# Kernel tuning notes

Measured on AMD Instinct MI355X. Metric: run time of the kernel, lower is better.

Reference implementation:

```python
import jax, jax.numpy as jnp
import numpy as np

B, S, H = 4, 2048, 1024
NH, HD = 16, 64
FF = 4 * H
EPS = 1e-5


def _layernorm(x, g, b):
    m = jnp.mean(x, axis=-1, keepdims=True)
    v = jnp.mean((x - m) ** 2, axis=-1, keepdims=True)
    return (x - m) * jax.lax.rsqrt(v + EPS) * g + b


def setup_inputs() -> dict:
    key = jax.random.key(0)
    ks = jax.random.split(key, 12)
    std = 1.0 / np.sqrt(H)
    inp = {
        "x": jax.random.normal(ks[0], (B, S, H), dtype=jnp.float32),
        "attention_mask": jnp.ones((B, S), dtype=bool),
        "Wq": jax.random.normal(ks[1], (H, H), dtype=jnp.float32) * std,
        "bq": jnp.zeros((H,), dtype=jnp.float32),
        "Wk": jax.random.normal(ks[2], (H, H), dtype=jnp.float32) * std,
        "bk": jnp.zeros((H,), dtype=jnp.float32),
        "Wv": jax.random.normal(ks[3], (H, H), dtype=jnp.float32) * std,
        "bv": jnp.zeros((H,), dtype=jnp.float32),
        "Wo": jax.random.normal(ks[4], (H, H), dtype=jnp.float32) * std,
        "bo": jnp.zeros((H,), dtype=jnp.float32),
        "g1": jnp.ones((H,), dtype=jnp.float32),
        "b1": jnp.zeros((H,), dtype=jnp.float32),
        "g2": jnp.ones((H,), dtype=jnp.float32),
        "b2": jnp.zeros((H,), dtype=jnp.float32),
        "Wm1": jax.random.normal(ks[5], (FF, H), dtype=jnp.float32) * std,
        "bm1": jnp.zeros((FF,), dtype=jnp.float32),
        "Wm2": jax.random.normal(ks[6], (H, FF), dtype=jnp.float32) * (1.0 / np.sqrt(FF)),
        "bm2": jnp.zeros((H,), dtype=jnp.float32),
    }
    return inp


def reference(x, attention_mask, Wq, bq, Wk, bk, Wv, bv, Wo, bo,
              g1, b1, g2, b2, Wm1, bm1, Wm2, bm2):
    scale = 1.0 / np.sqrt(HD)
    normed = _layernorm(x, g1, b1)
    # torch Linear: y = x @ W.T + b
    q = (normed @ Wq.T + bq).reshape(B, S, NH, HD)
    k = (normed @ Wk.T + bk).reshape(B, S, NH, HD)
    v = (normed @ Wv.T + bv).reshape(B, S, NH, HD)
    # scores: [B, NH, S, S]
    scores = jnp.einsum("bqhd,bkhd->bhqk", q, k) * scale
    scores = jnp.where(attention_mask[:, None, None, :], scores, -jnp.inf)
    attn = jax.nn.softmax(scores, axis=-1)
    out = jnp.einsum("bhqk,bkhd->bqhd", attn, v).reshape(B, S, H)
    out = out @ Wo.T + bo
    x = x + out
    h = _layernorm(x, g2, b2)
    h = jax.nn.gelu(h @ Wm1.T + bm1, approximate=False) @ Wm2.T + bm2
    return x + h
```

## Files before the change

kernel.cpp:

```cpp
#include <hip/hip_runtime.h>
#include <math.h>


typedef unsigned short u16;
typedef unsigned int   u32;
typedef __attribute__((ext_vector_type(4)))  float f32x4;
typedef __attribute__((ext_vector_type(16))) float f32x16;
typedef __attribute__((ext_vector_type(8)))  short short8;

__device__ __forceinline__ u16 f2bf(float f){
  union { float f; u32 u; } v; v.f = f;
  u32 u = v.u;
  return (u16)((u + 0x7fffu + ((u >> 16) & 1u)) >> 16);
}
__device__ __forceinline__ float bf2f(u16 h){
  union { u32 u; float f; } v; v.u = ((u32)h) << 16;
  return v.f;
}

__device__ __forceinline__ void async16(const u16* g, u16* l){
  __builtin_amdgcn_global_load_lds((const __attribute__((address_space(1))) u32*)g,
                                   (__attribute__((address_space(3))) u32*)l, 16, 0, 0);
}

__device__ __forceinline__ u32 cvt_pk_bf16(float lo, float hi){
  u32 r;
  asm("v_cvt_pk_bf16_f32 %0, %1, %2" : "=v"(r) : "v"(lo), "v"(hi));
  return r;
}

__device__ __forceinline__ short8 frag4(u32 a, u32 b, u32 c, u32 d){
  union { u32 u[4]; short8 s; } x;
  x.u[0] = a; x.u[1] = b; x.u[2] = c; x.u[3] = d;
  return x.s;
}

__global__ __launch_bounds__(256) void k_cvt(const float* __restrict__ src,
                                             u16* __restrict__ dst, int n){
  int i = (blockIdx.x * 256 + threadIdx.x) * 4;
  int stride = gridDim.x * 1024;
  for (; i < n; i += stride){
    float4 v = *(const float4*)(src + i);
    ushort4 o;
    o.x = f2bf(v.x); o.y = f2bf(v.y); o.z = f2bf(v.z); o.w = f2bf(v.w);
    *(ushort4*)(dst + i) = o;
  }
}

__global__ __launch_bounds__(256) void k_bias3(const float* __restrict__ a,
                                               const float* __restrict__ b,
                                               const float* __restrict__ c,
                                               float* __restrict__ o){
  int t = blockIdx.x * 256 + threadIdx.x;
  float v = t < 1024 ? a[t] : (t < 2048 ? b[t - 1024] : c[t - 2048]);
  o[t] = v;
}

__global__ __launch_bounds__(256) void k_ln(const float* __restrict__ x,
                                            const float* __restrict__ g,
                                            const float* __restrict__ b,
                                            u16* __restrict__ out){
  int row = blockIdx.x;
  int t = threadIdx.x;
  const float* xr = x + (size_t)row * 1024;
  float4 v = ((const float4*)xr)[t];
  float s = v.x + v.y + v.z + v.w;
  float q = v.x*v.x + v.y*v.y + v.z*v.z + v.w*v.w;
  #pragma unroll
  for (int off = 1; off < 64; off <<= 1){
    s += __shfl_xor(s, off);
    q += __shfl_xor(q, off);
  }
  __shared__ float ps[4], pq[4];
  int w = t >> 6, l = t & 63;
  if (l == 0){ ps[w] = s; pq[w] = q; }
  __syncthreads();
  s = ps[0] + ps[1] + ps[2] + ps[3];
  q = pq[0] + pq[1] + pq[2] + pq[3];
  float mean = s * (1.0f/1024.0f);
  float var  = q * (1.0f/1024.0f) - mean*mean;
  float rstd = rsqrtf(var + 1e-5f);
  float4 gv = ((const float4*)g)[t];
  float4 bv = ((const float4*)b)[t];
  ushort4 o;
  o.x = f2bf((v.x - mean)*rstd*gv.x + bv.x);
  o.y = f2bf((v.y - mean)*rstd*gv.y + bv.y);
  o.z = f2bf((v.z - mean)*rstd*gv.z + bv.z);
  o.w = f2bf((v.w - mean)*rstd*gv.w + bv.w);
  ((ushort4*)(out + (size_t)row * 1024))[t] = o;
}

#define MF(FRB, FCB) { \
  _Pragma("unroll") for (int ks = 0; ks < 2; ks++) \
  _Pragma("unroll") for (int fr = 0; fr < 4; fr++) \
  _Pragma("unroll") for (int fc = 0; fc < 2; fc++) \
    acc[(FRB)+fr][(FCB)+fc] = __builtin_amdgcn_mfma_f32_16x16x32_bf16( \
        a[fr][ks], b[fc][ks], acc[(FRB)+fr][(FCB)+fc], 0, 0, 0); }

#define STAGE(BUF, H, KT) { \
  async16(hbase[H] + (size_t)gr_[0]*K + (KT)*64 + gc_[0], &lds[BUF][H][t*8]); \
  async16(hbase[H] + (size_t)gr_[1]*K + (KT)*64 + gc_[1], &lds[BUF][H][4096 + t*8]); }

#define BARRIER() { __builtin_amdgcn_s_barrier(); __builtin_amdgcn_sched_barrier(0); }

template<int EPI>
__global__ __launch_bounds__(512, 2) void k_gemm256(const u16* __restrict__ A,
    const u16* __restrict__ Bw, const float* __restrict__ bias, void* __restrict__ Cp,
    const float* __restrict__ res, int M, int N, int K, int ntn){
  __shared__ __align__(16) u16 lds[2][4][8192];
  const int t = threadIdx.x;
  const int l = t & 63, w = t >> 6;
  const int wm = w >> 2, wn = w & 3;
  const int lr = l & 15, g = l >> 4;

  const int nwg = gridDim.x;
  int wg = blockIdx.x;
  if (!(nwg & 7)) wg = (wg & 7) * (nwg >> 3) + (wg >> 3);
  const int bm = (wg / ntn) * 256, bn = (wg % ntn) * 256;

  int gr_[2], gc_[2];
  #pragma unroll
  for (int i = 0; i < 2; i++){
    int ch = i*512 + t;
    int sr = ch >> 7, sc = (ch >> 6) & 1, r = (ch >> 2) & 15;
    int c  = ((ch & 3) * 8) ^ (((r >> 3) & 1) << 4);
    gr_[i] = sr*16 + r;
    gc_[i] = sc*32 + c;
  }
  const u16* hbase[4] = { A  + (size_t) bm        * K,
                          A  + (size_t)(bm + 128) * K,
                          Bw + (size_t) bn        * K,
                          Bw + (size_t)(bn + 128) * K };

  const int roff = lr*32 + ((g*8) ^ (((lr >> 3) & 1) << 4));

  f32x4 acc[8][4];
  #pragma unroll
  for (int i = 0; i < 8; i++)
    #pragma unroll
    for (int j = 0; j < 4; j++)
      acc[i][j] = (f32x4)(0.0f);
  short8 a[4][2], b[2][2];

  #define LDA(HB) { _Pragma("unroll") for (int fr = 0; fr < 4; fr++) \
    _Pragma("unroll") for (int ks = 0; ks < 2; ks++) \
      a[fr][ks] = *(const short8*)((HB) + (fr*4 + wm*2 + ks)*512 + roff); }
  #define LDB(HB) { _Pragma("unroll") for (int fc = 0; fc < 2; fc++) \
    _Pragma("unroll") for (int ks = 0; ks < 2; ks++) \
      b[fc][ks] = *(const short8*)((HB) + ((fc*4 + wn)*2 + ks)*512 + roff); }

  const int NT = K >> 6;
  STAGE(0, 0, 0); STAGE(0, 2, 0); STAGE(0, 3, 0); STAGE(0, 1, 0);
  asm volatile("s_waitcnt vmcnt(4)" ::: "memory");
  BARRIER();

  for (int kt = 0; kt < NT; kt++){
    const int cu = kt & 1, nx = cu ^ 1;
    const u16* LA0 = lds[cu][0]; const u16* LA1 = lds[cu][1];
    const u16* LB0 = lds[cu][2]; const u16* LB1 = lds[cu][3];
    const bool pf = (kt + 1 < NT);
    LDA(LA0); LDB(LB0);
    if (pf) STAGE(nx, 0, kt+1);
    __builtin_amdgcn_s_setprio(1);
    MF(0, 0);
    __builtin_amdgcn_s_setprio(0);
    if (pf) asm volatile("s_waitcnt vmcnt(4)" ::: "memory");
    else    asm volatile("s_waitcnt vmcnt(2)" ::: "memory");
    BARRIER();
    LDB(LB1);
    if (pf) STAGE(nx, 2, kt+1);
    __builtin_amdgcn_s_setprio(1);
    MF(0, 2);
    __builtin_amdgcn_s_setprio(0);
    if (pf) asm volatile("s_waitcnt vmcnt(4)" ::: "memory");
    else    asm volatile("s_waitcnt vmcnt(0)" ::: "memory");
    BARRIER();
    LDA(LA1);
    if (pf) STAGE(nx, 3, kt+1);
    __builtin_amdgcn_s_setprio(1);
    MF(4, 2);
    __builtin_amdgcn_s_setprio(0);
    BARRIER();
    LDB(LB0);
    if (pf) STAGE(nx, 1, kt+1);
    __builtin_amdgcn_s_setprio(1);
    MF(4, 0);
    __builtin_amdgcn_s_setprio(0);
    if (pf) asm volatile("s_waitcnt vmcnt(4)" ::: "memory");
    BARRIER();
  }

  const int m0 = bm + wm*16 + g*4;
  const int n0 = bn + wn*16 + lr;
  #pragma unroll
  for (int fc = 0; fc < 4; fc++){
    int col = n0 + fc*64;
    float bb = bias[col];
    #pragma unroll
    for (int fr = 0; fr < 8; fr++){
      int rowb = m0 + fr*32;
      #pragma unroll
      for (int r = 0; r < 4; r++){
        float v = acc[fr][fc][r] + bb;
        if constexpr (EPI == 2)
          v = 0.5f * v * (1.0f + erff(v * 0.70710678118654752f));
        size_t idx = (size_t)(rowb + r) * N + col;
        if constexpr (EPI == 1)
          ((float*)Cp)[idx] = v + res[idx];
        else
          ((u16*)Cp)[idx] = f2bf(v);
      }
    }
  }
}
#undef MF
#undef STAGE
#undef LDA
#undef LDB
#undef BARRIER

__global__ __launch_bounds__(256) void k_flash(const u16* __restrict__ QKV,
                                               u16* __restrict__ O){
  constexpr int QSTR = 3072, OSTR = 1024;
  __shared__ __align__(16) u16 lK [2][64*64];
  __shared__ __align__(16) u16 lVT[2][64*64];

  const int t = threadIdx.x;
  const int l = t & 63, w = t >> 6;
  const int c31 = l & 31, h = l >> 5;
  const int bx = blockIdx.x;
  const int qt = bx & 15, bh = bx >> 4;
  const size_t rowbase = (size_t)(bh >> 4) * 2048;
  const int hd = (bh & 15) * 64;
  const u16* Qg = QKV + rowbase * QSTR + hd;
  const u16* Kg = Qg + 1024;
  const u16* Vg = Qg + 2048;
  u16* Og = O + rowbase * OSTR + hd;
  const int qrow0 = qt * 128 + w * 32;

  short8 qf[4];
  #pragma unroll
  for (int d0 = 0; d0 < 4; d0++){
    short8 v = *(const short8*)(Qg + (size_t)(qrow0 + c31) * QSTR + d0*16 + 8*h);
    #pragma unroll
    for (int j = 0; j < 8; j++)
      v[j] = (short)f2bf(bf2f((u16)v[j]) * 0.125f);
    qf[d0] = v;
  }

  f32x16 oa0 = (f32x16)(0.0f), oa1 = (f32x16)(0.0f);
  float m_run = -1e30f, l_run = 0.0f;

  const int vkv0 = 2*(t & 31), vdh = t >> 5;
  const int rb = (c31 & 7) << 4;

  {
    #pragma unroll
    for (int i = 0; i < 2; i++){
      int idx = i*256 + t;
      int row = idx >> 3, c = (idx & 7) ^ (row & 7);
      async16(Kg + (size_t)row * QSTR + c*8, &lK[0][idx*8]);
    }
    const u16* vs = Vg + (size_t)vkv0 * QSTR + vdh*8;
    short8 v0 = *(const short8*)(vs);
    short8 v1 = *(const short8*)(vs + QSTR);
    #pragma unroll
    for (int i = 0; i < 8; i++){
      int d = vdh*8 + i;
      u32 word = (u32)(u16)v0[i] | ((u32)(u16)v1[i] << 16);
      *(u32*)((char*)&lVT[0][0] + d*128 + ((vkv0*2) ^ ((d&7)<<4))) = word;
    }
  }
  __syncthreads();

  short8 v0s, v1s;
  for (int kt = 0; kt < 32; kt++){
    const int cur = kt & 1;
    const char* lKc = (const char*)&lK[cur][0];
    const char* lVc = (const char*)&lVT[cur][0];

    if (kt < 31){
      #pragma unroll
      for (int i = 0; i < 2; i++){
        int idx = i*256 + t;
        int row = idx >> 3, c = (idx & 7) ^ (row & 7);
        async16(Kg + (size_t)((kt+1)*64 + row) * QSTR + c*8, &lK[cur^1][idx*8]);
      }
      const u16* vs = Vg + (size_t)((kt+1)*64 + vkv0) * QSTR + vdh*8;
      v0s = *(const short8*)(vs);
      v1s = *(const short8*)(vs + QSTR);
    }

    f32x16 sa0 = (f32x16)(0.0f), sa1 = (f32x16)(0.0f);
    #pragma unroll
    for (int d0 = 0; d0 < 4; d0++){
      int cb = (d0*32 + 16*h) ^ rb;
      short8 kf0 = *(const short8*)(lKc + c31*128 + cb);
      short8 kf1 = *(const short8*)(lKc + (32+c31)*128 + cb);
      sa0 = __builtin_amdgcn_mfma_f32_32x32x16_bf16(kf0, qf[d0], sa0, 0, 0, 0);
      sa1 = __builtin_amdgcn_mfma_f32_32x32x16_bf16(kf1, qf[d0], sa1, 0, 0, 0);
    }

    float pm = fmaxf(sa0[0], sa0[1]);
    #pragma unroll
    for (int r = 2; r < 16; r++) pm = fmaxf(pm, sa0[r]);
    #pragma unroll
    for (int r = 0; r < 16; r++) pm = fmaxf(pm, sa1[r]);
    pm = fmaxf(pm, __shfl_xor(pm, 32));
    if (!__all(pm <= m_run + 8.0f)){
      float mnew = fmaxf(m_run, pm);
      float alpha = __expf(m_run - mnew);
      m_run = mnew;
      l_run *= alpha;
      #pragma unroll
      for (int r = 0; r < 16; r++){
        int qr = (r&3) + 8*(r>>2) + 4*h;
        float ar = __shfl(alpha, qr);
        oa0[r] *= ar; oa1[r] *= ar;
      }
    }
    float rs = 0.0f;
    #pragma unroll
    for (int r = 0; r < 16; r++){ float p = __expf(sa0[r] - m_run); sa0[r] = p; rs += p; }
    #pragma unroll
    for (int r = 0; r < 16; r++){ float p = __expf(sa1[r] - m_run); sa1[r] = p; rs += p; }
    rs += __shfl_xor(rs, 32);
    l_run += rs;

    short8 pa[4];
    {
      u32 a0 = cvt_pk_bf16(sa0[0], sa0[1]),  a1 = cvt_pk_bf16(sa0[2], sa0[3]);
      u32 a2 = cvt_pk_bf16(sa0[4], sa0[5]),  a3 = cvt_pk_bf16(sa0[6], sa0[7]);
      asm("v_permlane32_swap_b32 %0, %1" : "+v"(a0), "+v"(a2));
      asm("v_permlane32_swap_b32 %0, %1" : "+v"(a1), "+v"(a3));
      pa[0] = frag4(a0, a1, a2, a3);
      u32 b0 = cvt_pk_bf16(sa0[8], sa0[9]),  b1 = cvt_pk_bf16(sa0[10], sa0[11]);
      u32 b2 = cvt_pk_bf16(sa0[12], sa0[13]), b3 = cvt_pk_bf16(sa0[14], sa0[15]);
      asm("v_permlane32_swap_b32 %0, %1" : "+v"(b0), "+v"(b2));
      asm("v_permlane32_swap_b32 %0, %1" : "+v"(b1), "+v"(b3));
      pa[1] = frag4(b0, b1, b2, b3);
      u32 c0 = cvt_pk_bf16(sa1[0], sa1[1]),  c1 = cvt_pk_bf16(sa1[2], sa1[3]);
      u32 c2 = cvt_pk_bf16(sa1[4], sa1[5]),  c3 = cvt_pk_bf16(sa1[6], sa1[7]);
      asm("v_permlane32_swap_b32 %0, %1" : "+v"(c0), "+v"(c2));
      asm("v_permlane32_swap_b32 %0, %1" : "+v"(c1), "+v"(c3));
      pa[2] = frag4(c0, c1, c2, c3);
      u32 d0 = cvt_pk_bf16(sa1[8], sa1[9]),  d1 = cvt_pk_bf16(sa1[10], sa1[11]);
      u32 d2 = cvt_pk_bf16(sa1[12], sa1[13]), d3 = cvt_pk_bf16(sa1[14], sa1[15]);
      asm("v_permlane32_swap_b32 %0, %1" : "+v"(d0), "+v"(d2));
      asm("v_permlane32_swap_b32 %0, %1" : "+v"(d1), "+v"(d3));
      pa[3] = frag4(d0, d1, d2, d3);
    }

    #pragma unroll
    for (int ks = 0; ks < 4; ks++){
      int cb = (ks*32 + 16*h) ^ rb;
      short8 vb0 = *(const short8*)(lVc + c31*128 + cb);
      short8 vb1 = *(const short8*)(lVc + (32+c31)*128 + cb);
      oa0 = __builtin_amdgcn_mfma_f32_32x32x16_bf16(pa[ks], vb0, oa0, 0, 0, 0);
      oa1 = __builtin_amdgcn_mfma_f32_32x32x16_bf16(pa[ks], vb1, oa1, 0, 0, 0);
    }

    if (kt < 31){
      #pragma unroll
      for (int i = 0; i < 8; i++){
        int d = vdh*8 + i;
        u32 word = (u32)(u16)v0s[i] | ((u32)(u16)v1s[i] << 16);
        *(u32*)((char*)&lVT[cur^1][0] + d*128 + ((vkv0*2) ^ ((d&7)<<4))) = word;
      }
    }
    __syncthreads();
  }

  float linv = 1.0f / l_run;
  #pragma unroll
  for (int r = 0; r < 16; r++){
    int qr = (r&3) + 8*(r>>2) + 4*h;
    float lr2 = __shfl(linv, qr);
    size_t ro = (size_t)(qrow0 + qr) * OSTR;
    Og[ro + c31]      = f2bf(oa0[r] * lr2);
    Og[ro + 32 + c31] = f2bf(oa1[r] * lr2);
  }
}

extern "C" void kernel_launch(void* const* d_in, const int* in_sizes, int n_in,
                              void* d_out, int out_size, void* d_ws, size_t ws_size,
                              hipStream_t stream){
  const float* x   = (const float*)d_in[0];
  const float* Wq  = (const float*)d_in[2];
  const float* bq  = (const float*)d_in[3];
  const float* Wk  = (const float*)d_in[4];
  const float* bk  = (const float*)d_in[5];
  const float* Wv  = (const float*)d_in[6];
  const float* bv  = (const float*)d_in[7];
  const float* Wo  = (const float*)d_in[8];
  const float* bo  = (const float*)d_in[9];
  const float* g1  = (const float*)d_in[10];
  const float* b1  = (const float*)d_in[11];
  const float* g2  = (const float*)d_in[12];
  const float* b2  = (const float*)d_in[13];
  const float* Wm1 = (const float*)d_in[14];
  const float* bm1 = (const float*)d_in[15];
  const float* Wm2 = (const float*)d_in[16];
  const float* bm2 = (const float*)d_in[17];

  const size_t MB = 1024 * 1024;
  char* ws = (char*)d_ws;
  u16*   wqkv = (u16*)(ws + 0*MB);
  u16*   wo   = (u16*)(ws + 6*MB);
  u16*   wm1  = (u16*)(ws + 8*MB);
  u16*   wm2  = (u16*)(ws + 16*MB);
  float* bqkv = (float*)(ws + 24*MB);
  u16*   nrm  = (u16*)(ws + 25*MB);
  u16*   qkvb = (u16*)(ws + 41*MB);
  u16*   attn = (u16*)(ws + 89*MB);
  float* x2   = (float*)(ws + 105*MB);
  u16*   h1   = (u16*)(ws + 41*MB);

  k_cvt<<<1024, 256, 0, stream>>>(Wq,  wqkv,             1024*1024);
  k_cvt<<<1024, 256, 0, stream>>>(Wk,  wqkv + 1024*1024, 1024*1024);
  k_cvt<<<1024, 256, 0, stream>>>(Wv,  wqkv + 2048*1024, 1024*1024);
  k_cvt<<<1024, 256, 0, stream>>>(Wo,  wo,  1024*1024);
  k_cvt<<<4096, 256, 0, stream>>>(Wm1, wm1, 4096*1024);
  k_cvt<<<4096, 256, 0, stream>>>(Wm2, wm2, 4096*1024);
  k_bias3<<<12, 256, 0, stream>>>(bq, bk, bv, bqkv);

  const int M = 8192;
  k_ln<<<M, 256, 0, stream>>>(x, g1, b1, nrm);
  k_gemm256<0><<<dim3(32*12), 512, 0, stream>>>(nrm, wqkv, bqkv, qkvb, nullptr, M, 3072, 1024, 12);
  k_flash<<<1024, 256, 0, stream>>>(qkvb, attn);
  k_gemm256<1><<<dim3(32*4), 512, 0, stream>>>(attn, wo, bo, x2, x, M, 1024, 1024, 4);
  k_ln<<<M, 256, 0, stream>>>(x2, g2, b2, nrm);
  k_gemm256<2><<<dim3(32*16), 512, 0, stream>>>(nrm, wm1, bm1, h1, nullptr, M, 4096, 1024, 16);
  k_gemm256<1><<<dim3(32*4), 512, 0, stream>>>(h1, wm2, bm2, d_out, x2, M, 1024, 4096, 4);
}
```

Before: 454.6 us.

## Pre-transpose V in separate kernel, fuse weight conversions, use exp2 softmax

Adds a kernel that transposes V per head into a contiguous buffer, so the flash kernel can load V^T into LDS with async global-to-LDS copies instead of register loads plus scattered LDS stores. The seven weight and bias conversion launches are merged into one kernel. Softmax now uses exp2f, with the log2(e) factor folded into the Q scale. The cost is an extra pass over V and an extra buffer, plus an unused nrm2 pointer.

```diff
diff --git a/kernel.cpp b/kernel.cpp
--- a/kernel.cpp
+++ b/kernel.cpp
@@ -35,25 +35,31 @@
   return x.s;
 }
 
-__global__ __launch_bounds__(256) void k_cvt(const float* __restrict__ src,
-                                             u16* __restrict__ dst, int n){
-  int i = (blockIdx.x * 256 + threadIdx.x) * 4;
-  int stride = gridDim.x * 1024;
-  for (; i < n; i += stride){
-    float4 v = *(const float4*)(src + i);
-    ushort4 o;
-    o.x = f2bf(v.x); o.y = f2bf(v.y); o.z = f2bf(v.z); o.w = f2bf(v.w);
-    *(ushort4*)(dst + i) = o;
-  }
-}
-
-__global__ __launch_bounds__(256) void k_bias3(const float* __restrict__ a,
-                                               const float* __restrict__ b,
-                                               const float* __restrict__ c,
-                                               float* __restrict__ o){
-  int t = blockIdx.x * 256 + threadIdx.x;
-  float v = t < 1024 ? a[t] : (t < 2048 ? b[t - 1024] : c[t - 2048]);
-  o[t] = v;
+__global__ __launch_bounds__(256) void k_cvt_all(
+    const float* __restrict__ Wq, const float* __restrict__ Wk,
+    const float* __restrict__ Wv, const float* __restrict__ Wo,
+    const float* __restrict__ Wm1, const float* __restrict__ Wm2,
+    const float* __restrict__ bq, const float* __restrict__ bk,
+    const float* __restrict__ bv,
+    u16* __restrict__ wqkv, u16* __restrict__ wo,
+    u16* __restrict__ wm1, u16* __restrict__ wm2, float* __restrict__ bqkv){
+  int c = blockIdx.x * 256 + threadIdx.x;
+  const float* src; u16* dst;
+  if      (c <  262144){ src = Wq  + c*4;             dst = wqkv + c*4; }
+  else if (c <  524288){ src = Wk  + (c-262144)*4;    dst = wqkv + 1048576 + (c-262144)*4; }
+  else if (c <  786432){ src = Wv  + (c-524288)*4;    dst = wqkv + 2097152 + (c-524288)*4; }
+  else if (c < 1048576){ src = Wo  + (c-786432)*4;    dst = wo  + (c-786432)*4; }
+  else if (c < 2097152){ src = Wm1 + (c-1048576)*4;   dst = wm1 + (c-1048576)*4; }
+  else if (c < 3145728){ src = Wm2 + (c-2097152)*4;   dst = wm2 + (c-2097152)*4; }
+  else if (c < 3146496){
+    int i = (c - 3145728)*4;
+    const float* bsrc = i < 1024 ? bq + i : (i < 2048 ? bk + i - 1024 : bv + i - 2048);
+    *(float4*)(bqkv + i) = *(const float4*)bsrc;
+    return;
+  } else return;
+  float4 v = *(const float4*)src;
+  ushort4 o; o.x = f2bf(v.x); o.y = f2bf(v.y); o.z = f2bf(v.z); o.w = f2bf(v.w);
+  *(ushort4*)dst = o;
 }
 
 __global__ __launch_bounds__(256) void k_ln(const float* __restrict__ x,
@@ -88,6 +94,33 @@
   o.z = f2bf((v.z - mean)*rstd*gv.z + bv.z);
   o.w = f2bf((v.w - mean)*rstd*gv.w + bv.w);
   ((ushort4*)(out + (size_t)row * 1024))[t] = o;
+}
+
+__global__ __launch_bounds__(256) void k_vt(const u16* __restrict__ QKV,
+                                            u16* __restrict__ VT){
+  __shared__ u16 lt[64][66];
+  const int t = threadIdx.x;
+  const int bh = blockIdx.x >> 5, sblk = blockIdx.x & 31;
+  const size_t rowbase = (size_t)(bh >> 4) * 2048;
+  const int hd = (bh & 15) * 64;
+  const u16* src = QKV + (rowbase + sblk*64) * 3072 + hd + 2048;
+  u16* dst = VT + (size_t)bh * 131072 + sblk*64;
+  #pragma unroll
+  for (int i = 0; i < 2; i++){
+    int r = i*32 + (t >> 3), c0 = (t & 7) * 8;
+    short8 v = *(const short8*)(src + (size_t)r * 3072 + c0);
+    #pragma unroll
+    for (int j = 0; j < 8; j++) lt[r][c0 + j] = (u16)v[j];
+  }
+  __syncthreads();
+  #pragma unroll
+  for (int i = 0; i < 2; i++){
+    int d = i*32 + (t >> 3), toff = (t & 7) * 8;
+    short8 o;
+    #pragma unroll
+    for (int j = 0; j < 8; j++) o[j] = (short)lt[toff + j][d];
+    *(short8*)(dst + (size_t)d * 2048 + toff) = o;
+  }
 }
 
 #define MF(FRB, FCB) { \
@@ -220,6 +253,7 @@
 #undef BARRIER
 
 __global__ __launch_bounds__(256) void k_flash(const u16* __restrict__ QKV,
+                                               const u16* __restrict__ VT,
                                                u16* __restrict__ O){
   constexpr int QSTR = 3072, OSTR = 1024;
   __shared__ __align__(16) u16 lK [2][64*64];
@@ -232,9 +266,9 @@
   const int qt = bx & 15, bh = bx >> 4;
   const size_t rowbase = (size_t)(bh >> 4) * 2048;
   const int hd = (bh & 15) * 64;
-  const u16* Qg = QKV + rowbase * QSTR + hd;
-  const u16* Kg = Qg + 1024;
-  const u16* Vg = Qg + 2048;
+  const u16* Qg  = QKV + rowbase * QSTR + hd;
+  const u16* Kg  = Qg + 1024;
+  const u16* VTg = VT + (size_t)bh * 131072;
   u16* Og = O + rowbase * OSTR + hd;
   const int qrow0 = qt * 128 + w * 32;
 
@@ -244,36 +278,23 @@
     short8 v = *(const short8*)(Qg + (size_t)(qrow0 + c31) * QSTR + d0*16 + 8*h);
     #pragma unroll
     for (int j = 0; j < 8; j++)
-      v[j] = (short)f2bf(bf2f((u16)v[j]) * 0.125f);
+      v[j] = (short)f2bf(bf2f((u16)v[j]) * 0.18033688011112042f);
     qf[d0] = v;
   }
 
   f32x16 oa0 = (f32x16)(0.0f), oa1 = (f32x16)(0.0f);
   float m_run = -1e30f, l_run = 0.0f;
-
-  const int vkv0 = 2*(t & 31), vdh = t >> 5;
   const int rb = (c31 & 7) << 4;
 
-  {
-    #pragma unroll
-    for (int i = 0; i < 2; i++){
-      int idx = i*256 + t;
-      int row = idx >> 3, c = (idx & 7) ^ (row & 7);
-      async16(Kg + (size_t)row * QSTR + c*8, &lK[0][idx*8]);
-    }
-    const u16* vs = Vg + (size_t)vkv0 * QSTR + vdh*8;
-    short8 v0 = *(const short8*)(vs);
-    short8 v1 = *(const short8*)(vs + QSTR);
-    #pragma unroll
-    for (int i = 0; i < 8; i++){
-      int d = vdh*8 + i;
-      u32 word = (u32)(u16)v0[i] | ((u32)(u16)v1[i] << 16);
-      *(u32*)((char*)&lVT[0][0] + d*128 + ((vkv0*2) ^ ((d&7)<<4))) = word;
-    }
+  #pragma unroll
+  for (int i = 0; i < 2; i++){
+    int idx = i*256 + t;
+    int row = idx >> 3, c = (idx & 7) ^ (row & 7);
+    async16(Kg  + (size_t)row * QSTR + c*8, &lK [0][idx*8]);
+    async16(VTg + (size_t)row * 2048 + c*8, &lVT[0][idx*8]);
   }
   __syncthreads();
 
-  short8 v0s, v1s;
   for (int kt = 0; kt < 32; kt++){
     const int cur = kt & 1;
     const char* lKc = (const char*)&lK[cur][0];
@@ -284,11 +305,9 @@
       for (int i = 0; i < 2; i++){
         int idx = i*256 + t;
         int row = idx >> 3, c = (idx & 7) ^ (row & 7);
-        async16(Kg + (size_t)((kt+1)*64 + row) * QSTR + c*8, &lK[cur^1][idx*8]);
+        async16(Kg  + (size_t)((kt+1)*64 + row) * QSTR + c*8, &lK [cur^1][idx*8]);
+        async16(VTg + (size_t)row * 2048 + (kt+1)*64 + c*8,   &lVT[cur^1][idx*8]);
       }
-      const u16* vs = Vg + (size_t)((kt+1)*64 + vkv0) * QSTR + vdh*8;
-      v0s = *(const short8*)(vs);
-      v1s = *(const short8*)(vs + QSTR);
     }
 
     f32x16 sa0 = (f32x16)(0.0f), sa1 = (f32x16)(0.0f);
@@ -309,7 +328,7 @@
     pm = fmaxf(pm, __shfl_xor(pm, 32));
     if (!__all(pm <= m_run + 8.0f)){
       float mnew = fmaxf(m_run, pm);
-      float alpha = __expf(m_run - mnew);
+      float alpha = exp2f(m_run - mnew);
       m_run = mnew;
       l_run *= alpha;
       #pragma unroll
@@ -321,9 +340,9 @@
     }
     float rs = 0.0f;
     #pragma unroll
-    for (int r = 0; r < 16; r++){ float p = __expf(sa0[r] - m_run); sa0[r] = p; rs += p; }
-    #pragma unroll
-    for (int r = 0; r < 16; r++){ float p = __expf(sa1[r] - m_run); sa1[r] = p; rs += p; }
+    for (int r = 0; r < 16; r++){ float p = exp2f(sa0[r] - m_run); sa0[r] = p; rs += p; }
+    #pragma unroll
+    for (int r = 0; r < 16; r++){ float p = exp2f(sa1[r] - m_run); sa1[r] = p; rs += p; }
     rs += __shfl_xor(rs, 32);
     l_run += rs;
 
@@ -359,15 +378,6 @@
       oa0 = __builtin_amdgcn_mfma_f32_32x32x16_bf16(pa[ks], vb0, oa0, 0, 0, 0);
       oa1 = __builtin_amdgcn_mfma_f32_32x32x16_bf16(pa[ks], vb1, oa1, 0, 0, 0);
     }
-
-    if (kt < 31){
-      #pragma unroll
-      for (int i = 0; i < 8; i++){
-        int d = vdh*8 + i;
-        u32 word = (u32)(u16)v0s[i] | ((u32)(u16)v1s[i] << 16);
-        *(u32*)((char*)&lVT[cur^1][0] + d*128 + ((vkv0*2) ^ ((d&7)<<4))) = word;
-      }
-    }
     __syncthreads();
   }
 
@@ -411,23 +421,22 @@
   u16*   wm2  = (u16*)(ws + 16*MB);
   float* bqkv = (float*)(ws + 24*MB);
   u16*   nrm  = (u16*)(ws + 25*MB);
+  u16*   vt   = (u16*)(ws + 25*MB);
   u16*   qkvb = (u16*)(ws + 41*MB);
   u16*   attn = (u16*)(ws + 89*MB);
   float* x2   = (float*)(ws + 105*MB);
   u16*   h1   = (u16*)(ws + 41*MB);
-
-  k_cvt<<<1024, 256, 0, stream>>>(Wq,  wqkv,             1024*1024);
-  k_cvt<<<1024, 256, 0, stream>>>(Wk,  wqkv + 1024*1024, 1024*1024);
-  k_cvt<<<1024, 256, 0, stream>>>(Wv,  wqkv + 2048*1024, 1024*1024);
-  k_cvt<<<1024, 256, 0, stream>>>(Wo,  wo,  1024*1024);
-  k_cvt<<<4096, 256, 0, stream>>>(Wm1, wm1, 4096*1024);
-  k_cvt<<<4096, 256, 0, stream>>>(Wm2, wm2, 4096*1024);
-  k_bias3<<<12, 256, 0, stream>>>(bq, bk, bv, bqkv);
+  u16*   nrm2 = (u16*)(ws + 73*MB);
+
+
+  k_cvt_all<<<12291, 256, 0, stream>>>(Wq, Wk, Wv, Wo, Wm1, Wm2, bq, bk, bv,
+                                       wqkv, wo, wm1, wm2, bqkv);
 
   const int M = 8192;
   k_ln<<<M, 256, 0, stream>>>(x, g1, b1, nrm);
   k_gemm256<0><<<dim3(32*12), 512, 0, stream>>>(nrm, wqkv, bqkv, qkvb, nullptr, M, 3072, 1024, 12);
-  k_flash<<<1024, 256, 0, stream>>>(qkvb, attn);
+  k_vt<<<2048, 256, 0, stream>>>(qkvb, vt);
+  k_flash<<<1024, 256, 0, stream>>>(qkvb, vt, attn);
   k_gemm256<1><<<dim3(32*4), 512, 0, stream>>>(attn, wo, bo, x2, x, M, 1024, 1024, 4);
   k_ln<<<M, 256, 0, stream>>>(x2, g2, b2, nrm);
   k_gemm256<2><<<dim3(32*16), 512, 0, stream>>>(nrm, wm1, bm1, h1, nullptr, M, 4096, 1024, 16);
```

After: 467.0 us. 2.7% more time.
